# Performance work log

Hardware: AMD Instinct MI355X
Metric: run time of the kernel (lower is better)

Reference implementation:

```python
import jax, jax.numpy as jnp
import numpy as np

EMBED_DIM = 1024
N_HEAD = 16

def setup_inputs() -> dict:
    key = jax.random.key(0)
    ks = jax.random.split(key, 5)
    C = EMBED_DIM
    x = jax.random.normal(ks[0], (2, 2048, C), dtype=jnp.float32)
    s = 1.0 / np.sqrt(C)
    W_attn = jax.random.normal(ks[1], (C, 3 * C), dtype=jnp.float32) * s
    b_attn = jnp.zeros((3 * C,), dtype=jnp.float32)
    W_proj = jax.random.normal(ks[2], (C, C), dtype=jnp.float32) * s
    b_proj = jnp.zeros((C,), dtype=jnp.float32)
    return {"x": x, "W_attn": W_attn, "b_attn": b_attn, "W_proj": W_proj, "b_proj": b_proj}

def reference(x, W_attn, b_attn, W_proj, b_proj):
    B, T, C = x.shape
    H = N_HEAD
    D = C // H
    qkv = x @ W_attn + b_attn                      # [B,T,3C]
    q, k, v = jnp.split(qkv, 3, axis=-1)
    # [B,H,T,D]
    q = q.reshape(B, T, H, D).transpose(0, 2, 1, 3)
    k = k.reshape(B, T, H, D).transpose(0, 2, 1, 3)
    v = v.reshape(B, T, H, D).transpose(0, 2, 1, 3)
    att = jnp.einsum('bhqd,bhkd->bhqk', q, k) * (1.0 / jnp.sqrt(jnp.asarray(D, x.dtype)))
    causal = jnp.tril(jnp.ones((T, T), dtype=bool))
    att = jnp.where(causal, att, -jnp.inf)
    att = jax.nn.softmax(att, axis=-1)
    y = jnp.einsum('bhqk,bhkd->bhqd', att, v)      # [B,H,T,D]
    y = y.transpose(0, 2, 1, 3).reshape(B, T, C)
    return y @ W_proj + b_proj
```

## Files before the change

kernel.cpp:

```cpp
#include <hip/hip_runtime.h>
#include <stdint.h>

typedef __attribute__((ext_vector_type(4))) float f32x4;
typedef __attribute__((ext_vector_type(8))) __bf16 bf16x8;
typedef __attribute__((ext_vector_type(8))) unsigned short u16x8;

__device__ __forceinline__ unsigned short f2b(float f) {
  unsigned u = __float_as_uint(f);
  u += 0x7FFFu + ((u >> 16) & 1u);
  return (unsigned short)(u >> 16);
}

__device__ __forceinline__ void gload_lds16(const void* g, void* l) {
  typedef __attribute__((address_space(1))) void GV1;
  typedef __attribute__((address_space(3))) void LV3;
  __builtin_amdgcn_global_load_lds((GV1*)(void*)g, (LV3*)l, 16, 0, 0);
}

__global__ __launch_bounds__(256) void convert_f32_bf16(const float* __restrict__ in,
                                                        unsigned short* __restrict__ out, int n) {
  int i = (blockIdx.x * 256 + threadIdx.x) * 8;
  if (i >= n) return;
  float4 a = *(const float4*)(in + i);
  float4 b = *(const float4*)(in + i + 4);
  u16x8 r;
  r[0] = f2b(a.x); r[1] = f2b(a.y); r[2] = f2b(a.z); r[3] = f2b(a.w);
  r[4] = f2b(b.x); r[5] = f2b(b.y); r[6] = f2b(b.z); r[7] = f2b(b.w);
  *(u16x8*)(out + i) = r;
}

__global__ __launch_bounds__(256) void transpose_f32_bf16(const float* __restrict__ W,
                                                          unsigned short* __restrict__ Wt,
                                                          int K, int N) {
  __shared__ unsigned short tile[32][33];
  int n0 = blockIdx.x * 32, k0 = blockIdx.y * 32;
  int tx = threadIdx.x, ty = threadIdx.y;
  #pragma unroll
  for (int j = 0; j < 32; j += 8)
    tile[ty + j][tx] = f2b(W[(size_t)(k0 + ty + j) * N + n0 + tx]);
  __syncthreads();
  #pragma unroll
  for (int j = 0; j < 32; j += 8)
    Wt[(size_t)(n0 + ty + j) * K + k0 + tx] = tile[tx][ty + j];
}

template <bool OUT_BF16>
__global__ __launch_bounds__(256) void gemm_bt(const unsigned short* __restrict__ A,
                                               const unsigned short* __restrict__ Bt,
                                               const float* __restrict__ bias,
                                               void* __restrict__ Cout,
                                               int M, int N, int K) {
  __shared__ unsigned short As[128 * 64];
  __shared__ unsigned short Bs[128 * 64];
  const int m0 = blockIdx.x * 128, n0 = blockIdx.y * 128;
  const int tid = threadIdx.x;
  const int w = tid >> 6, l = tid & 63;
  const int wm = w >> 1, wn = w & 1;
  const int c = l & 15, g = l >> 4;
  f32x4 acc[4][4] = {};
  for (int k0 = 0; k0 < K; k0 += 64) {
    #pragma unroll
    for (int i = 0; i < 4; ++i) {
      int rb = w * 32 + i * 8;
      gload_lds16(A + (size_t)(m0 + rb + (l >> 3)) * K + k0 + (l & 7) * 8, &As[rb * 64]);
      gload_lds16(Bt + (size_t)(n0 + rb + (l >> 3)) * K + k0 + (l & 7) * 8, &Bs[rb * 64]);
    }
    __syncthreads();
    #pragma unroll
    for (int ks = 0; ks < 2; ++ks) {
      bf16x8 af[4], bf[4];
      #pragma unroll
      for (int mi = 0; mi < 4; ++mi)
        af[mi] = *(const bf16x8*)&As[(wm * 64 + mi * 16 + c) * 64 + ks * 32 + g * 8];
      #pragma unroll
      for (int ni = 0; ni < 4; ++ni)
        bf[ni] = *(const bf16x8*)&Bs[(wn * 64 + ni * 16 + c) * 64 + ks * 32 + g * 8];
      #pragma unroll
      for (int mi = 0; mi < 4; ++mi)
        #pragma unroll
        for (int ni = 0; ni < 4; ++ni)
          acc[mi][ni] = __builtin_amdgcn_mfma_f32_16x16x32_bf16(af[mi], bf[ni], acc[mi][ni], 0, 0, 0);
    }
    __syncthreads();
  }
  #pragma unroll
  for (int mi = 0; mi < 4; ++mi) {
    #pragma unroll
    for (int ni = 0; ni < 4; ++ni) {
      int colg = n0 + wn * 64 + ni * 16 + c;
      float bv = bias[colg];
      #pragma unroll
      for (int r = 0; r < 4; ++r) {
        int rowg = m0 + wm * 64 + mi * 16 + 4 * g + r;
        float v = acc[mi][ni][r] + bv;
        if (OUT_BF16)
          ((unsigned short*)Cout)[(size_t)rowg * N + colg] = f2b(v);
        else
          ((float*)Cout)[(size_t)rowg * N + colg] = v;
      }
    }
  }
}

__global__ __launch_bounds__(256) void attn_kernel(const unsigned short* __restrict__ qkv,
                                                   unsigned short* __restrict__ out) {
  __shared__ unsigned short K_lds[2][64 * 64];
  __shared__ unsigned short V_lds[2][64 * 64];
  __shared__ unsigned short P_lds[4 * 16 * 64];
  const int bid = blockIdx.x;
  const int qt = 31 - (bid >> 5);
  const int bh = bid & 31;
  const int b = bh >> 4, h = bh & 15;
  const int tid = threadIdx.x, w = tid >> 6, l = tid & 63;
  const int c = l & 15, g = l >> 4;
  const size_t row0 = (size_t)b * 2048;
  const int vp = tid & 31, vcb = tid >> 5;
  const float SCL = 0.18033688f;
  char* Pb = (char*)&P_lds[w * 16 * 64];

  const int q0 = qt * 64;
  const int q0w = q0 + w * 16;
  const int nt = qt + 1;

  bf16x8 qf[2];
  #pragma unroll
  for (int ks = 0; ks < 2; ++ks)
    qf[ks] = *(const bf16x8*)(qkv + (row0 + q0w + c) * 3072 + h * 64 + ks * 32 + g * 8);

  f32x4 acc[4] = {};
  float mstate[4], lstate[4];
  #pragma unroll
  for (int r = 0; r < 4; ++r) { mstate[r] = -1e30f; lstate[r] = 0.f; }

  {
    #pragma unroll
    for (int i = 0; i < 2; ++i) {
      int rb = w * 16 + i * 8;
      int row = rb + (l >> 3);
      int ch = (l & 7) ^ (row & 7);
      gload_lds16(qkv + (row0 + row) * 3072 + 1024 + h * 64 + ch * 8, &K_lds[0][rb * 64]);
    }
    size_t tr = row0 + 2 * vp;
    u16x8 v0 = *(const u16x8*)(qkv + tr * 3072 + 2048 + h * 64 + vcb * 8);
    u16x8 v1 = *(const u16x8*)(qkv + (tr + 1) * 3072 + 2048 + h * 64 + vcb * 8);
    char* Vb = (char*)V_lds[0];
    #pragma unroll
    for (int j = 0; j < 8; ++j) {
      int d = vcb * 8 + j;
      int off = d * 128 + ((4 * vp) ^ ((d & 7) << 4));
      *(unsigned int*)(Vb + off) = (unsigned int)v0[j] | ((unsigned int)v1[j] << 16);
    }
  }
  __syncthreads();

  for (int t = 0; t < nt; ++t) {
    const int cur = t & 1;
    const int kv0 = t * 64;
    const bool pre = (t + 1 < nt);
    u16x8 v0n, v1n;
    if (pre) {
      const int kvn = kv0 + 64;
      #pragma unroll
      for (int i = 0; i < 2; ++i) {
        int rb = w * 16 + i * 8;
        int row = rb + (l >> 3);
        int ch = (l & 7) ^ (row & 7);
        gload_lds16(qkv + (row0 + kvn + row) * 3072 + 1024 + h * 64 + ch * 8,
                    &K_lds[cur ^ 1][rb * 64]);
      }
      size_t tr = row0 + kvn + 2 * vp;
      v0n = *(const u16x8*)(qkv + tr * 3072 + 2048 + h * 64 + vcb * 8);
      v1n = *(const u16x8*)(qkv + (tr + 1) * 3072 + 2048 + h * 64 + vcb * 8);
    }
    const char* Kb = (const char*)K_lds[cur];
    const char* Vb = (const char*)V_lds[cur];
    f32x4 s[4] = {};
    #pragma unroll
    for (int ks = 0; ks < 2; ++ks) {
      bf16x8 kf[4];
      #pragma unroll
      for (int nk = 0; nk < 4; ++nk) {
        int row = nk * 16 + c;
        kf[nk] = *(const bf16x8*)(Kb + row * 128 + ((ks * 64 + g * 16) ^ ((row & 7) << 4)));
      }
      __builtin_amdgcn_s_setprio(1);
      #pragma unroll
      for (int nk = 0; nk < 4; ++nk)
        s[nk] = __builtin_amdgcn_mfma_f32_16x16x32_bf16(qf[ks], kf[nk], s[nk], 0, 0, 0);
      __builtin_amdgcn_s_setprio(0);
    }
    if (t == nt - 1) {
      #pragma unroll
      for (int nk = 0; nk < 4; ++nk)
        #pragma unroll
        for (int r = 0; r < 4; ++r) {
          int rowg = q0w + 4 * g + r;
          int colg = kv0 + nk * 16 + c;
          if (colg > rowg) s[nk][r] = -1e30f;
        }
    }
    #pragma unroll
    for (int r = 0; r < 4; ++r) {
      float mx = fmaxf(fmaxf(s[0][r], s[1][r]), fmaxf(s[2][r], s[3][r]));
      mx = fmaxf(mx, __shfl_xor(mx, 1));
      mx = fmaxf(mx, __shfl_xor(mx, 2));
      mx = fmaxf(mx, __shfl_xor(mx, 4));
      mx = fmaxf(mx, __shfl_xor(mx, 8));
      float mold = mstate[r];
      float mnew = fmaxf(mold, mx);
      float alpha = exp2f((mold - mnew) * SCL);
      mstate[r] = mnew;
      float ms = mnew * SCL;
      float rs = 0.f;
      #pragma unroll
      for (int nk = 0; nk < 4; ++nk) {
        float p = exp2f(fmaf(s[nk][r], SCL, -ms));
        s[nk][r] = p;
        rs += p;
      }
      rs += __shfl_xor(rs, 1);
      rs += __shfl_xor(rs, 2);
      rs += __shfl_xor(rs, 4);
      rs += __shfl_xor(rs, 8);
      lstate[r] = lstate[r] * alpha + rs;
      #pragma unroll
      for (int nd = 0; nd < 4; ++nd) acc[nd][r] *= alpha;
    }
    #pragma unroll
    for (int nk = 0; nk < 4; ++nk)
      #pragma unroll
      for (int r = 0; r < 4; ++r) {
        int row = 4 * g + r;
        int off = row * 128 + (((nk * 16 + c) * 2) ^ ((row & 7) << 4));
        *(unsigned short*)(Pb + off) = f2b(s[nk][r]);
      }
    #pragma unroll
    for (int ks = 0; ks < 2; ++ks) {
      bf16x8 pf, vf[4];
      pf = *(const bf16x8*)(Pb + c * 128 + ((ks * 64 + g * 16) ^ ((c & 7) << 4)));
      #pragma unroll
      for (int nd = 0; nd < 4; ++nd) {
        int row = nd * 16 + c;
        vf[nd] = *(const bf16x8*)(Vb + row * 128 + ((ks * 64 + g * 16) ^ ((row & 7) << 4)));
      }
      __builtin_amdgcn_s_setprio(1);
      #pragma unroll
      for (int nd = 0; nd < 4; ++nd)
        acc[nd] = __builtin_amdgcn_mfma_f32_16x16x32_bf16(pf, vf[nd], acc[nd], 0, 0, 0);
      __builtin_amdgcn_s_setprio(0);
    }
    if (pre) {
      char* Vbn = (char*)V_lds[cur ^ 1];
      #pragma unroll
      for (int j = 0; j < 8; ++j) {
        int d = vcb * 8 + j;
        int off = d * 128 + ((4 * vp) ^ ((d & 7) << 4));
        *(unsigned int*)(Vbn + off) = (unsigned int)v0n[j] | ((unsigned int)v1n[j] << 16);
      }
    }
    __syncthreads();
  }
  #pragma unroll
  for (int r = 0; r < 4; ++r) {
    float rinv = 1.0f / lstate[r];
    size_t t = row0 + q0w + 4 * g + r;
    #pragma unroll
    for (int nd = 0; nd < 4; ++nd)
      out[t * 1024 + h * 64 + nd * 16 + c] = f2b(acc[nd][r] * rinv);
  }
}

extern "C" void kernel_launch(void* const* d_in, const int* in_sizes, int n_in,
                              void* d_out, int out_size, void* d_ws, size_t ws_size,
                              hipStream_t stream) {
  const float* x      = (const float*)d_in[0];
  const float* W_attn = (const float*)d_in[1];
  const float* b_attn = (const float*)d_in[2];
  const float* W_proj = (const float*)d_in[3];
  const float* b_proj = (const float*)d_in[4];
  float* out = (float*)d_out;

  char* ws = (char*)d_ws;
  unsigned short* x_bf     = (unsigned short*)(ws + 0);
  unsigned short* Wattn_t  = (unsigned short*)(ws + 8388608);
  unsigned short* Wproj_t  = (unsigned short*)(ws + 14680064);
  unsigned short* qkv      = (unsigned short*)(ws + 16777216);
  unsigned short* attn_out = (unsigned short*)(ws + 41943040);

  convert_f32_bf16<<<2048, 256, 0, stream>>>(x, x_bf, 4194304);
  transpose_f32_bf16<<<dim3(96, 32), dim3(32, 8), 0, stream>>>(W_attn, Wattn_t, 1024, 3072);
  transpose_f32_bf16<<<dim3(32, 32), dim3(32, 8), 0, stream>>>(W_proj, Wproj_t, 1024, 1024);

  gemm_bt<true><<<dim3(32, 24), 256, 0, stream>>>(x_bf, Wattn_t, b_attn, qkv, 4096, 3072, 1024);
  attn_kernel<<<1024, 256, 0, stream>>>(qkv, attn_out);
  gemm_bt<false><<<dim3(32, 8), 256, 0, stream>>>(attn_out, Wproj_t, b_proj, out, 4096, 1024, 1024);
}
```

Baseline: 163.6 us.

## Balance causal tile scheduling and skip redundant online-softmax rescaling

Remaps block IDs so each group of blocks pairs short and long causal query tiles (qt and 31-qt), which evens out per-block work across the grid. The online softmax now skips the alpha rescale of the accumulator and l when no row max grew anywhere in the wavefront. It also keeps per-lane partial row sums and reduces them with shuffles only once at the end, instead of every tile. This removes per-tile shuffles and exp work, at the cost of a wave-uniform branch and a different block ordering that may change cache locality.

```diff
diff --git a/kernel.cpp b/kernel.cpp
--- a/kernel.cpp
+++ b/kernel.cpp
@@ -108,8 +108,10 @@
   __shared__ unsigned short V_lds[2][64 * 64];
   __shared__ unsigned short P_lds[4 * 16 * 64];
   const int bid = blockIdx.x;
-  const int qt = 31 - (bid >> 5);
-  const int bh = bid & 31;
+  const int p = bid & 255, j = bid >> 8;
+  const int bh = p & 31;
+  const int v2 = 2 * (p >> 5);
+  const int qt = (j & 1) ? (31 - v2 - (j >> 1)) : (v2 + (j >> 1));
   const int b = bh >> 4, h = bh & 15;
   const int tid = threadIdx.x, w = tid >> 6, l = tid & 63;
   const int c = l & 15, g = l >> 4;
@@ -145,10 +147,10 @@
     u16x8 v1 = *(const u16x8*)(qkv + (tr + 1) * 3072 + 2048 + h * 64 + vcb * 8);
     char* Vb = (char*)V_lds[0];
     #pragma unroll
-    for (int j = 0; j < 8; ++j) {
-      int d = vcb * 8 + j;
+    for (int jj = 0; jj < 8; ++jj) {
+      int d = vcb * 8 + jj;
       int off = d * 128 + ((4 * vp) ^ ((d & 7) << 4));
-      *(unsigned int*)(Vb + off) = (unsigned int)v0[j] | ((unsigned int)v1[j] << 16);
+      *(unsigned int*)(Vb + off) = (unsigned int)v0[jj] | ((unsigned int)v1[jj] << 16);
     }
   }
   __syncthreads();
@@ -199,32 +201,39 @@
           if (colg > rowg) s[nk][r] = -1e30f;
         }
     }
+    float mx[4];
     #pragma unroll
     for (int r = 0; r < 4; ++r) {
-      float mx = fmaxf(fmaxf(s[0][r], s[1][r]), fmaxf(s[2][r], s[3][r]));
-      mx = fmaxf(mx, __shfl_xor(mx, 1));
-      mx = fmaxf(mx, __shfl_xor(mx, 2));
-      mx = fmaxf(mx, __shfl_xor(mx, 4));
-      mx = fmaxf(mx, __shfl_xor(mx, 8));
-      float mold = mstate[r];
-      float mnew = fmaxf(mold, mx);
-      float alpha = exp2f((mold - mnew) * SCL);
-      mstate[r] = mnew;
-      float ms = mnew * SCL;
-      float rs = 0.f;
-      #pragma unroll
-      for (int nk = 0; nk < 4; ++nk) {
-        float p = exp2f(fmaf(s[nk][r], SCL, -ms));
-        s[nk][r] = p;
-        rs += p;
-      }
-      rs += __shfl_xor(rs, 1);
-      rs += __shfl_xor(rs, 2);
-      rs += __shfl_xor(rs, 4);
-      rs += __shfl_xor(rs, 8);
-      lstate[r] = lstate[r] * alpha + rs;
-      #pragma unroll
-      for (int nd = 0; nd < 4; ++nd) acc[nd][r] *= alpha;
+      float m0 = fmaxf(fmaxf(s[0][r], s[1][r]), fmaxf(s[2][r], s[3][r]));
+      m0 = fmaxf(m0, __shfl_xor(m0, 1));
+      m0 = fmaxf(m0, __shfl_xor(m0, 2));
+      m0 = fmaxf(m0, __shfl_xor(m0, 4));
+      m0 = fmaxf(m0, __shfl_xor(m0, 8));
+      mx[r] = m0;
+    }
+    bool nogrow = (mx[0] <= mstate[0]) & (mx[1] <= mstate[1]) &
+                  (mx[2] <= mstate[2]) & (mx[3] <= mstate[3]);
+    if (!__all(nogrow)) {
+      #pragma unroll
+      for (int r = 0; r < 4; ++r) {
+        float mold = mstate[r];
+        float mnew = fmaxf(mold, mx[r]);
+        float alpha = exp2f((mold - mnew) * SCL);
+        mstate[r] = mnew;
+        lstate[r] *= alpha;
+        #pragma unroll
+        for (int nd = 0; nd < 4; ++nd) acc[nd][r] *= alpha;
+      }
+    }
+    #pragma unroll
+    for (int r = 0; r < 4; ++r) {
+      float ms = mstate[r] * SCL;
+      float p0 = exp2f(fmaf(s[0][r], SCL, -ms));
+      float p1 = exp2f(fmaf(s[1][r], SCL, -ms));
+      float p2 = exp2f(fmaf(s[2][r], SCL, -ms));
+      float p3 = exp2f(fmaf(s[3][r], SCL, -ms));
+      s[0][r] = p0; s[1][r] = p1; s[2][r] = p2; s[3][r] = p3;
+      lstate[r] += (p0 + p1) + (p2 + p3);
     }
     #pragma unroll
     for (int nk = 0; nk < 4; ++nk)
@@ -252,17 +261,22 @@
     if (pre) {
       char* Vbn = (char*)V_lds[cur ^ 1];
       #pragma unroll
-      for (int j = 0; j < 8; ++j) {
-        int d = vcb * 8 + j;
+      for (int jj = 0; jj < 8; ++jj) {
+        int d = vcb * 8 + jj;
         int off = d * 128 + ((4 * vp) ^ ((d & 7) << 4));
-        *(unsigned int*)(Vbn + off) = (unsigned int)v0n[j] | ((unsigned int)v1n[j] << 16);
+        *(unsigned int*)(Vbn + off) = (unsigned int)v0n[jj] | ((unsigned int)v1n[jj] << 16);
       }
     }
     __syncthreads();
   }
   #pragma unroll
   for (int r = 0; r < 4; ++r) {
-    float rinv = 1.0f / lstate[r];
+    float ls = lstate[r];
+    ls += __shfl_xor(ls, 1);
+    ls += __shfl_xor(ls, 2);
+    ls += __shfl_xor(ls, 4);
+    ls += __shfl_xor(ls, 8);
+    float rinv = 1.0f / ls;
     size_t t = row0 + q0w + 4 * g + r;
     #pragma unroll
     for (int nd = 0; nd < 4; ++nd)
```

New measurement: 174.8 us. 1.07x slower.
